# Kernel tuning notes

Hardware: AMD Instinct MI355X
Metric: run time of the kernel (lower is better)

Reference implementation:

```python
import jax, jax.numpy as jnp
import numpy as np

N = 100000     # total points
PBS = 500      # point_batch_size (hard-coded in module)
K = 100        # num_neighbors
KP = 15        # num_kernel_points
EPS = 1e-5


def _bn(x, g, b, axes):
    # torch BatchNorm in training mode: batch stats, biased variance
    m = jnp.mean(x, axis=axes, keepdims=True)
    v = jnp.var(x, axis=axes, keepdims=True)
    return (x - m) / jnp.sqrt(v + EPS) * g + b


def setup_inputs() -> dict:
    key = jax.random.key(0)
    ks = jax.random.split(key, 16)
    rn = lambda k, sh, s=1.0: jax.random.normal(k, sh, jnp.float32) * s
    return {
        "pts": rn(ks[0], (N, 3)),
        "normal": rn(ks[1], (N, 3)),
        "kp_points": rn(ks[2], (KP, 3)),
        "kp_weights": rn(ks[3], (KP, 3, 128), 0.3),
        "kp_sigma": jnp.float32(1.0),
        "conv1_w": rn(ks[4], (1024, 128), 128 ** -0.5),
        "conv1_b": rn(ks[5], (1024,), 0.02),
        "bn1_g": jnp.ones((1024,), jnp.float32),
        "bn1_b": jnp.zeros((1024,), jnp.float32),
        "fc1_w": rn(ks[6], (512, 1024), 1024 ** -0.5),
        "fc1_b": rn(ks[7], (512,), 0.02),
        "bn4_g": jnp.ones((512,), jnp.float32),
        "bn4_b": jnp.zeros((512,), jnp.float32),
        "fc2_w": rn(ks[8], (256, 512), 512 ** -0.5),
        "fc2_b": rn(ks[9], (256,), 0.02),
        "bn5_g": jnp.ones((256,), jnp.float32),
        "bn5_b": jnp.zeros((256,), jnp.float32),
        "fc3_w": rn(ks[10], (3, 256), 256 ** -0.5),
        "fc3_b": rn(ks[11], (3,), 0.02),
        "index": jax.random.randint(ks[12], (PBS,), 0, N, jnp.int32),
    }


def reference(pts, normal, kp_points, kp_weights, kp_sigma,
              conv1_w, conv1_b, bn1_g, bn1_b,
              fc1_w, fc1_b, bn4_g, bn4_b,
              fc2_w, fc2_b, bn5_g, bn5_b,
              fc3_w, fc3_b, index):
    sel = pts[index]                                               # [B,3]
    # L-inf pairwise distance and kNN (topk of -dist, as in the torch code)
    dist = jnp.max(jnp.abs(sel[:, None, :] - pts[None, :, :]), axis=-1)  # [B,N]
    _, nbr = jax.lax.top_k(-dist, K)                               # [B,K]
    rel = pts[nbr] - sel[:, None, :]                               # [B,K,3]

    # KPConv: gaussian weights vs kernel points, per-kernel-point linear map
    d2 = jnp.sum((rel[:, :, None, :] - kp_points[None, None]) ** 2, axis=-1)  # [B,K,KP]
    w = jnp.exp(-0.5 * d2 / (kp_sigma ** 2))
    wf = rel[:, :, None, :] * w[..., None]                         # [B,K,KP,3]
    h = jax.nn.relu(jnp.einsum('bnkc,kco->bno', wf, kp_weights))   # [B,K,128]

    # 1x1 conv 128->1024, relu then BN over (batch, points) per channel
    h = jnp.einsum('bnc,oc->bno', h, conv1_w) + conv1_b            # [B,K,1024]
    h = _bn(jax.nn.relu(h), bn1_g, bn1_b, (0, 1))
    feat = jnp.max(h, axis=1)                                      # [B,1024]

    feat = _bn(jax.nn.relu(feat @ fc1_w.T + fc1_b), bn4_g, bn4_b, (0,))
    feat = _bn(jax.nn.relu(feat @ fc2_w.T + fc2_b), bn5_g, bn5_b, (0,))
    feat = feat @ fc3_w.T + fc3_b                                  # [B,3]
    return feat, normal[index]
```

## Files before the change

### kernel.cpp

```cpp
#include <hip/hip_runtime.h>
#include <hip/hip_fp16.h>

#define NPTS 100000
#define NB 500
#define KNN 100
#define KPN 15
#define C1 128
#define C2 1024
#define C3 512
#define C4 256

#define G 64
#define NCELLS (G * G * G)
#define GB 5.0f
#define GINVH ((float)G / (2.f * GB))
#define CAND_CAP 2048

typedef _Float16 half8 __attribute__((ext_vector_type(8)));
typedef float f32x4 __attribute__((ext_vector_type(4)));

__device__ __forceinline__ int cell_coord(float x) {
  int c = (int)floorf((x + GB) * GINVH);
  return min(max(c, 0), G - 1);
}
__device__ __forceinline__ int cell_of(float x, float y, float z) {
  return (cell_coord(x) << 12) | (cell_coord(y) << 6) | cell_coord(z);
}

__global__ __launch_bounds__(256) void prep_kernel(
    const float* __restrict__ pts, const float* __restrict__ normal,
    const int* __restrict__ index, const float* __restrict__ w1,
    const float* __restrict__ kpw, const float* __restrict__ fc1w,
    float* __restrict__ sel, float* __restrict__ out2,
    __half* __restrict__ wh, __half* __restrict__ kpwT_hi,
    __half* __restrict__ kpwT_lo, __half* __restrict__ fwhi,
    __half* __restrict__ fwlo, unsigned* __restrict__ cnt) {
  int i = blockIdx.x * 256 + threadIdx.x;
  if (i < NB) {
    int ix = index[i];
    sel[i * 3 + 0] = pts[3 * ix + 0];
    sel[i * 3 + 1] = pts[3 * ix + 1];
    sel[i * 3 + 2] = pts[3 * ix + 2];
    out2[i * 3 + 0] = normal[3 * ix + 0];
    out2[i * 3 + 1] = normal[3 * ix + 1];
    out2[i * 3 + 2] = normal[3 * ix + 2];
  }
  if (i < C2 * C1) wh[i] = __float2half(w1[i]);
  if (i < 128 * 64) {
    int o = i >> 6, j = i & 63;
    float v = (j < 45) ? kpw[j * 128 + o] : 0.f;
    __half hi = __float2half_rn(v);
    kpwT_hi[i] = hi;
    kpwT_lo[i] = __float2half_rn(v - __half2float(hi));
  }
  if (i < C3 * C2) {
    float v = fc1w[i];
    __half hi = __float2half_rn(v);
    fwhi[i] = hi;
    fwlo[i] = __float2half_rn(v - __half2float(hi));
  }
  if (i < NPTS)
    atomicAdd(&cnt[cell_of(pts[3 * i], pts[3 * i + 1], pts[3 * i + 2])], 1u);
}

__global__ __launch_bounds__(256) void grid_scan1_kernel(
    const unsigned* __restrict__ cnt, unsigned* __restrict__ cursor,
    unsigned* __restrict__ chunktot) {
  const int tid = threadIdx.x;
  int base = blockIdx.x * 1024 + tid * 4;
  unsigned c0 = cnt[base], c1 = cnt[base + 1], c2 = cnt[base + 2],
           c3 = cnt[base + 3];
  unsigned tot = c0 + c1 + c2 + c3;
  __shared__ unsigned sb[256];
  sb[tid] = tot;
  __syncthreads();
  for (int off = 1; off < 256; off <<= 1) {
    unsigned add = (tid >= off) ? sb[tid - off] : 0u;
    __syncthreads();
    sb[tid] += add;
    __syncthreads();
  }
  unsigned excl = sb[tid] - tot;
  cursor[base] = excl;
  cursor[base + 1] = excl + c0;
  cursor[base + 2] = excl + c0 + c1;
  cursor[base + 3] = excl + c0 + c1 + c2;
  if (tid == 255) chunktot[blockIdx.x] = sb[255];
}

__global__ __launch_bounds__(256) void grid_scan2_kernel(
    const unsigned* __restrict__ chunktot, unsigned* __restrict__ chunkoff) {
  const int tid = threadIdx.x;
  unsigned v = chunktot[tid];
  __shared__ unsigned sb[256];
  sb[tid] = v;
  __syncthreads();
  for (int off = 1; off < 256; off <<= 1) {
    unsigned add = (tid >= off) ? sb[tid - off] : 0u;
    __syncthreads();
    sb[tid] += add;
    __syncthreads();
  }
  chunkoff[tid] = sb[tid] - v;
}

__global__ __launch_bounds__(256) void grid_scan3_kernel(
    unsigned* __restrict__ cursor, const unsigned* __restrict__ chunkoff) {
  unsigned off = chunkoff[blockIdx.x];
  int base = blockIdx.x * 1024 + threadIdx.x * 4;
#pragma unroll
  for (int j = 0; j < 4; ++j) cursor[base + j] += off;
}

__global__ __launch_bounds__(256) void grid_scatter_kernel(
    const float* __restrict__ pts, unsigned* __restrict__ cursor,
    float4* __restrict__ sorted) {
  int i = blockIdx.x * 256 + threadIdx.x;
  if (i >= NPTS) return;
  float x = pts[3 * i], y = pts[3 * i + 1], z = pts[3 * i + 2];
  unsigned pos = atomicAdd(&cursor[cell_of(x, y, z)], 1u);
  sorted[pos] = make_float4(x, y, z, __int_as_float(i));
}

__device__ __forceinline__ unsigned linf_bits(float px, float py, float pz,
                                              float sx, float sy, float sz) {
  float dx = fabsf(px - sx), dy = fabsf(py - sy), dz = fabsf(pz - sz);
  return __float_as_uint(fmaxf(fmaxf(dx, dy), dz));
}

__global__ __launch_bounds__(256) void knn_kernel(
    const float4* __restrict__ sorted, const unsigned* __restrict__ cnt,
    const unsigned* __restrict__ cursor,
    const float* __restrict__ sel, int* __restrict__ nbr) {
  const int b = blockIdx.x;
  const int tid = threadIdx.x;
  __shared__ unsigned cbits[CAND_CAP];
  __shared__ int cidx[CAND_CAP];
  __shared__ unsigned hist[4096];
  __shared__ unsigned scanbuf[256];
  __shared__ int s_total, s_m, s_mc, s_chunk;
  __shared__ unsigned s_excl, s_bub;

  const float qx = sel[b * 3 + 0], qy = sel[b * 3 + 1], qz = sel[b * 3 + 2];
  const int qcx = cell_coord(qx), qcy = cell_coord(qy), qcz = cell_coord(qz);

  if (tid == 0) s_total = 0;
  __syncthreads();
  int s = 1;
  int pxlo = 1, pxhi = 0, pylo = 1, pyhi = 0, pzlo = 1, pzhi = 0;
  int xlo, xhi, ylo, yhi, zlo, zhi;
  for (;;) {
    xlo = max(qcx - s, 0); xhi = min(qcx + s, G - 1);
    ylo = max(qcy - s, 0); yhi = min(qcy + s, G - 1);
    zlo = max(qcz - s, 0); zhi = min(qcz + s, G - 1);
    int nx = xhi - xlo + 1, ny = yhi - ylo + 1, nz = zhi - zlo + 1;
    int ncell = nx * ny * nz;
    unsigned local = 0;
    for (int ci = tid; ci < ncell; ci += 256) {
      int cz = ci % nz;
      int r = ci / nz;
      int cy = r % ny;
      int cx = r / ny;
      int ax = xlo + cx, ay = ylo + cy, az = zlo + cz;
      if (ax >= pxlo && ax <= pxhi && ay >= pylo && ay <= pyhi &&
          az >= pzlo && az <= pzhi)
        continue;
      local += cnt[(ax << 12) | (ay << 6) | az];
    }
#pragma unroll
    for (int off = 32; off; off >>= 1) local += __shfl_down(local, off);
    if ((tid & 63) == 0) atomicAdd(&s_total, (int)local);
    __syncthreads();
    if (s_total >= KNN || (xlo == 0 && ylo == 0 && zlo == 0 && xhi == G - 1 &&
                           yhi == G - 1 && zhi == G - 1))
      break;
    pxlo = xlo; pxhi = xhi; pylo = ylo; pyhi = yhi; pzlo = zlo; pzhi = zhi;
    ++s;
    __syncthreads();
  }

  if (tid == 0) s_m = 0;
  __syncthreads();
  {
    int nx = xhi - xlo + 1, ny = yhi - ylo + 1, nz = zhi - zlo + 1;
    int ncell = nx * ny * nz;
    for (int ci = tid; ci < ncell; ci += 256) {
      int cz = ci % nz;
      int r = ci / nz;
      int cy = r % ny;
      int cx = r / ny;
      int cell = ((xlo + cx) << 12) | ((ylo + cy) << 6) | (zlo + cz);
      unsigned end = cursor[cell];
      unsigned beg = end - cnt[cell];
      int k = (int)(end - beg);
      if (k > 0) {
        int e0 = atomicAdd(&s_m, k);
        for (unsigned p = beg; p < end; ++p, ++e0) {
          if (e0 < CAND_CAP) {
            float4 f = sorted[p];
            cbits[e0] = linf_bits(f.x, f.y, f.z, qx, qy, qz);
            cidx[e0] = __float_as_int(f.w);
          }
        }
      }
    }
  }
  __syncthreads();
  int m = s_m < CAND_CAP ? s_m : CAND_CAP;

  for (int j = tid; j < 4096; j += 256) hist[j] = 0;
  __syncthreads();
  for (int e = tid; e < m; e += 256) atomicAdd(&hist[cbits[e] >> 19], 1u);
  __syncthreads();
  unsigned csum = 0;
  {
    int c0 = tid * 16;
#pragma unroll
    for (int j = 0; j < 16; ++j) csum += hist[c0 + j];
  }
  scanbuf[tid] = csum;
  __syncthreads();
  for (int off = 1; off < 256; off <<= 1) {
    unsigned add = (tid >= off) ? scanbuf[tid - off] : 0u;
    __syncthreads();
    scanbuf[tid] += add;
    __syncthreads();
  }
  {
    unsigned incl = scanbuf[tid], excl = incl - csum;
    if (excl < KNN && KNN <= incl) {
      s_chunk = tid;
      s_excl = excl;
    }
  }
  __syncthreads();
  if (tid == 0) {
    unsigned cum = s_excl;
    int bin = s_chunk * 16;
    while (cum + hist[bin] < KNN) {
      cum += hist[bin];
      ++bin;
    }
    s_bub = (unsigned)(bin + 1) << 19;
  }
  __syncthreads();

  const unsigned bub = s_bub;
  const float dub = __uint_as_float(bub);
  if (tid == 0) s_mc = 0;
  __syncthreads();
  {
    int xlo2 = min(max((int)floorf((qx - dub + GB) * GINVH), 0), G - 1);
    int xhi2 = min(max((int)floorf((qx + dub + GB) * GINVH), 0), G - 1);
    int ylo2 = min(max((int)floorf((qy - dub + GB) * GINVH), 0), G - 1);
    int yhi2 = min(max((int)floorf((qy + dub + GB) * GINVH), 0), G - 1);
    int zlo2 = min(max((int)floorf((qz - dub + GB) * GINVH), 0), G - 1);
    int zhi2 = min(max((int)floorf((qz + dub + GB) * GINVH), 0), G - 1);
    int nx = xhi2 - xlo2 + 1, ny = yhi2 - ylo2 + 1, nz = zhi2 - zlo2 + 1;
    int ncell = nx * ny * nz;
    for (int ci = tid; ci < ncell; ci += 256) {
      int cz = ci % nz;
      int r = ci / nz;
      int cy = r % ny;
      int cx = r / ny;
      int cell = ((xlo2 + cx) << 12) | ((ylo2 + cy) << 6) | (zlo2 + cz);
      unsigned end = cursor[cell];
      unsigned beg = end - cnt[cell];
      for (unsigned p = beg; p < end; ++p) {
        float4 f = sorted[p];
        unsigned bits = linf_bits(f.x, f.y, f.z, qx, qy, qz);
        if (bits < bub) {
          int e = atomicAdd(&s_mc, 1);
          if (e < CAND_CAP) {
            cbits[e] = bits;
            cidx[e] = __float_as_int(f.w);
          }
        }
      }
    }
  }
  __syncthreads();
  int mc = s_mc < CAND_CAP ? s_mc : CAND_CAP;

  for (int c = tid; c < mc; c += 256) {
    unsigned bc = cbits[c];
    int ic = cidx[c];
    int rank = 0;
    for (int j = 0; j < mc; ++j) {
      unsigned bj = cbits[j];
      rank += (bj < bc || (bj == bc && cidx[j] < ic)) ? 1 : 0;
    }
    if (rank < KNN) nbr[b * KNN + rank] = ic;
  }
}

__global__ __launch_bounds__(512) void kpconv_conv1_kernel(
    const float* __restrict__ pts, const float* __restrict__ sel,
    const int* __restrict__ nbr, const float* __restrict__ kp_points,
    const __half* __restrict__ kpwT_hi, const __half* __restrict__ kpwT_lo,
    const float* __restrict__ kp_sigma, const __half* __restrict__ wh,
    const float* __restrict__ bias, float* __restrict__ featmax,
    float* __restrict__ featmin, float* __restrict__ bnsum,
    float* __restrict__ bnsq) {
  const int b = blockIdx.x;
  const int tid = threadIdx.x;
  const int wave = tid >> 6, lane = tid & 63;
  const int lr = lane & 15, quad = lane >> 4;

  __shared__ __align__(16) char smem[71168];
  __half* As_hi = (__half*)smem;
  __half* As_lo = As_hi + 112 * 72;
  __half* Bs_hi = As_lo + 112 * 72;
  __half* Bs_lo = Bs_hi + 128 * 72;
  float* rel = (float*)(Bs_lo + 128 * 72);
  float* kpp = rel + 100 * 4;
  __half* Hs = (__half*)smem;
  __half* Ws = Hs + 112 * 136;

  for (int i = tid; i < 128 * 8; i += 512) {
    int row = i >> 3, seg = i & 7;
    *(float4*)&Bs_hi[row * 72 + seg * 8] =
        *(const float4*)&kpwT_hi[row * 64 + seg * 8];
    *(float4*)&Bs_lo[row * 72 + seg * 8] =
        *(const float4*)&kpwT_lo[row * 64 + seg * 8];
  }
  {
    float4 z = make_float4(0.f, 0.f, 0.f, 0.f);
    for (int i = tid; i < 112 * 8; i += 512) {
      int row = i >> 3, seg = i & 7;
      *(float4*)&As_hi[row * 72 + seg * 8] = z;
      *(float4*)&As_lo[row * 72 + seg * 8] = z;
    }
  }
  if (tid < 45) kpp[tid] = kp_points[tid];
  if (tid < 100) {
    int idx = nbr[b * KNN + tid];
    rel[tid * 4 + 0] = pts[3 * idx + 0] - sel[b * 3 + 0];
    rel[tid * 4 + 1] = pts[3 * idx + 1] - sel[b * 3 + 1];
    rel[tid * 4 + 2] = pts[3 * idx + 2] - sel[b * 3 + 2];
  }
  __syncthreads();

  const float sg = kp_sigma[0];
  const float inv2s2 = -0.5f / (sg * sg);
  for (int i = tid; i < 100 * KPN; i += 512) {
    int k = i / KPN, p = i - k * KPN;
    float rx = rel[k * 4 + 0] - kpp[p * 3 + 0];
    float ry = rel[k * 4 + 1] - kpp[p * 3 + 1];
    float rz = rel[k * 4 + 2] - kpp[p * 3 + 2];
    float w = expf(inv2s2 * (rx * rx + ry * ry + rz * rz));
#pragma unroll
    for (int c = 0; c < 3; ++c) {
      float a = rel[k * 4 + c] * w;
      __half hi = __float2half_rn(a);
      As_hi[k * 72 + p * 3 + c] = hi;
      As_lo[k * 72 + p * 3 + c] = __float2half_rn(a - __half2float(hi));
    }
  }
  __syncthreads();

  f32x4 acc1[7];
#pragma unroll
  for (int m = 0; m < 7; ++m) acc1[m] = (f32x4)(0.f);
#pragma unroll
  for (int s = 0; s < 2; ++s) {
    int boff = (wave * 16 + lr) * 72 + s * 32 + quad * 8;
    half8 bhi = *(const half8*)&Bs_hi[boff];
    half8 blo = *(const half8*)&Bs_lo[boff];
#pragma unroll
    for (int m = 0; m < 7; ++m) {
      int aoff = (m * 16 + lr) * 72 + s * 32 + quad * 8;
      half8 ahi = *(const half8*)&As_hi[aoff];
      half8 alo = *(const half8*)&As_lo[aoff];
      acc1[m] = __builtin_amdgcn_mfma_f32_16x16x32_f16(ahi, bhi, acc1[m], 0, 0, 0);
      acc1[m] = __builtin_amdgcn_mfma_f32_16x16x32_f16(ahi, blo, acc1[m], 0, 0, 0);
      acc1[m] = __builtin_amdgcn_mfma_f32_16x16x32_f16(alo, bhi, acc1[m], 0, 0, 0);
    }
  }
  __syncthreads();

  {
    int col = wave * 16 + lr;
#pragma unroll
    for (int m = 0; m < 7; ++m)
#pragma unroll
      for (int r = 0; r < 4; ++r) {
        int row = m * 16 + quad * 4 + r;
        Hs[row * 136 + col] = __float2half_rn(fmaxf(acc1[m][r], 0.f));
      }
  }

  for (int c = 0; c < 8; ++c) {
    __syncthreads();
    for (int i = tid; i < 128 * 16; i += 512) {
      int row = i >> 4, seg = i & 15;
      *(float4*)&Ws[row * 136 + seg * 8] =
          *(const float4*)&wh[(c * 128 + row) * 128 + seg * 8];
    }
    __syncthreads();

    f32x4 acc2[7];
#pragma unroll
    for (int m = 0; m < 7; ++m) acc2[m] = (f32x4)(0.f);
#pragma unroll
    for (int s = 0; s < 4; ++s) {
      half8 bfrag =
          *(const half8*)&Ws[(wave * 16 + lr) * 136 + s * 32 + quad * 8];
#pragma unroll
      for (int m = 0; m < 7; ++m) {
        half8 afrag =
            *(const half8*)&Hs[(m * 16 + lr) * 136 + s * 32 + quad * 8];
        acc2[m] = __builtin_amdgcn_mfma_f32_16x16x32_f16(afrag, bfrag,
                                                         acc2[m], 0, 0, 0);
      }
    }

    {
      int col = c * 128 + wave * 16 + lr;
      float bv = bias[col];
      float pmax = -1e30f, pmin = 1e30f, psum = 0.f, psq = 0.f;
#pragma unroll
      for (int m = 0; m < 7; ++m)
#pragma unroll
        for (int r = 0; r < 4; ++r) {
          int row = m * 16 + quad * 4 + r;
          if (row < 100) {
            float y = fmaxf(acc2[m][r] + bv, 0.f);
            pmax = fmaxf(pmax, y);
            pmin = fminf(pmin, y);
            psum += y;
            psq += y * y;
          }
        }
      pmax = fmaxf(pmax, __shfl_xor(pmax, 16));
      pmax = fmaxf(pmax, __shfl_xor(pmax, 32));
      pmin = fminf(pmin, __shfl_xor(pmin, 16));
      pmin = fminf(pmin, __shfl_xor(pmin, 32));
      psum += __shfl_xor(psum, 16);
      psum += __shfl_xor(psum, 32);
      psq += __shfl_xor(psq, 16);
      psq += __shfl_xor(psq, 32);
      if (quad == 0) {
        featmax[b * C2 + col] = pmax;
        featmin[b * C2 + col] = pmin;
        atomicAdd(&bnsum[col], psum);
        atomicAdd(&bnsq[col], psq);
      }
    }
  }
}

__global__ __launch_bounds__(256) void bn1half_kernel(
    const float* __restrict__ featmax, const float* __restrict__ featmin,
    const float* __restrict__ bnsum, const float* __restrict__ bnsq,
    const float* __restrict__ g, const float* __restrict__ bb,
    __half* __restrict__ Xhi, __half* __restrict__ Xlo) {
  int idx = blockIdx.x * 256 + threadIdx.x;
  if (idx >= NB * C2) return;
  int o = idx & (C2 - 1);
  const float invn = 1.f / (float)(NB * KNN);
  float m = bnsum[o] * invn;
  float v = bnsq[o] * invn - m * m;
  float a = g[o] / sqrtf(v + 1e-5f);
  float x = (a >= 0.f) ? featmax[idx] : featmin[idx];
  float y = (x - m) * a + bb[o];
  __half hi = __float2half_rn(y);
  Xhi[idx] = hi;
  Xlo[idx] = __float2half_rn(y - __half2float(hi));
}

__global__ __launch_bounds__(256) void fc1_mfma_kernel(
    const __half* __restrict__ Xhi, const __half* __restrict__ Xlo,
    const __half* __restrict__ Whi, const __half* __restrict__ Wlo,
    const float* __restrict__ bias, float* __restrict__ yraw,
    float* __restrict__ s, float* __restrict__ sq) {
  const int r0 = blockIdx.x * 64;
  const int n0 = blockIdx.y * 64;
  const int tid = threadIdx.x;
  const int wave = tid >> 6, lane = tid & 63;
  const int lr = lane & 15, quad = lane >> 4;
  __shared__ __half Xs_hi[64 * 72], Xs_lo[64 * 72];
  __shared__ __half Ws_hi[64 * 72], Ws_lo[64 * 72];

  f32x4 acc[4];
#pragma unroll
  for (int m = 0; m < 4; ++m) acc[m] = (f32x4)(0.f);

  for (int kc = 0; kc < C2; kc += 64) {
    __syncthreads();
    for (int i = tid; i < 64 * 8; i += 256) {
      int row = i >> 3, seg = i & 7;
      int gr = r0 + row;
      float4 vhi = make_float4(0.f, 0.f, 0.f, 0.f), vlo = vhi;
      if (gr < NB) {
        vhi = *(const float4*)&Xhi[gr * C2 + kc + seg * 8];
        vlo = *(const float4*)&Xlo[gr * C2 + kc + seg * 8];
      }
      *(float4*)&Xs_hi[row * 72 + seg * 8] = vhi;
      *(float4*)&Xs_lo[row * 72 + seg * 8] = vlo;
      *(float4*)&Ws_hi[row * 72 + seg * 8] =
          *(const float4*)&Whi[(n0 + row) * C2 + kc + seg * 8];
      *(float4*)&Ws_lo[row * 72 + seg * 8] =
          *(const float4*)&Wlo[(n0 + row) * C2 + kc + seg * 8];
    }
    __syncthreads();

#pragma unroll
    for (int s2 = 0; s2 < 2; ++s2) {
      int boff = (wave * 16 + lr) * 72 + s2 * 32 + quad * 8;
      half8 bhi = *(const half8*)&Ws_hi[boff];
      half8 blo = *(const half8*)&Ws_lo[boff];
#pragma unroll
      for (int m = 0; m < 4; ++m) {
        int aoff = (m * 16 + lr) * 72 + s2 * 32 + quad * 8;
        half8 ahi = *(const half8*)&Xs_hi[aoff];
        half8 alo = *(const half8*)&Xs_lo[aoff];
        acc[m] = __builtin_amdgcn_mfma_f32_16x16x32_f16(ahi, bhi, acc[m], 0, 0, 0);
        acc[m] = __builtin_amdgcn_mfma_f32_16x16x32_f16(ahi, blo, acc[m], 0, 0, 0);
        acc[m] = __builtin_amdgcn_mfma_f32_16x16x32_f16(alo, bhi, acc[m], 0, 0, 0);
      }
    }
  }

  {
    int col = n0 + wave * 16 + lr;
    float bv = bias[col];
    float psum = 0.f, psq = 0.f;
#pragma unroll
    for (int m = 0; m < 4; ++m)
#pragma unroll
      for (int r = 0; r < 4; ++r) {
        int row = r0 + m * 16 + quad * 4 + r;
        if (row < NB) {
          float y = fmaxf(acc[m][r] + bv, 0.f);
          yraw[row * C3 + col] = y;
          psum += y;
          psq += y * y;
        }
      }
    psum += __shfl_xor(psum, 16);
    psum += __shfl_xor(psum, 32);
    psq += __shfl_xor(psq, 16);
    psq += __shfl_xor(psq, 32);
    if (quad == 0) {
      atomicAdd(&s[col], psum);
      atomicAdd(&sq[col], psq);
    }
  }
}

__global__ __launch_bounds__(256) void fc2_kernel(
    const float* __restrict__ x,
    const float* __restrict__ bnsum, const float* __restrict__ bnsq,
    const float* __restrict__ g, const float* __restrict__ bb,
    const float* __restrict__ w,
    const float* __restrict__ bias, float* __restrict__ yraw,
    float* __restrict__ s, float* __restrict__ sq) {
  const int r0 = blockIdx.x * 4;
  const int n0 = blockIdx.y * 64;
  const int tid = threadIdx.x;
  const int col = tid >> 2;
  const int row = tid & 3;
  __shared__ float xs[4][516];
  __shared__ float ws[64][132];
  __shared__ float amul[C3], badd[C3];
  const float invn = 1.f / (float)NB;
  for (int o = tid; o < C3; o += 256) {
    float m = bnsum[o] * invn;
    float v = bnsq[o] * invn - m * m;
    float a = g[o] / sqrtf(v + 1e-5f);
    amul[o] = a;
    badd[o] = bb[o] - m * a;
  }
  __syncthreads();
  for (int f = tid; f < C3; f += 256) {
    int rr = f >> 7, kq = (f & 127) * 4;
    float4 xv = *(const float4*)&x[(r0 + rr) * C3 + kq];
    float4 o4;
    o4.x = xv.x * amul[kq + 0] + badd[kq + 0];
    o4.y = xv.y * amul[kq + 1] + badd[kq + 1];
    o4.z = xv.z * amul[kq + 2] + badd[kq + 2];
    o4.w = xv.w * amul[kq + 3] + badd[kq + 3];
    *(float4*)&xs[rr][kq] = o4;
  }
  float acc = 0.f;
  for (int kc = 0; kc < C3; kc += 128) {
    __syncthreads();
#pragma unroll
    for (int i = 0; i < 8; ++i) {
      int f = tid + i * 256;
      int cr = f >> 5, kq = (f & 31) * 4;
      *(float4*)&ws[cr][kq] = *(const float4*)&w[(n0 + cr) * C3 + kc + kq];
    }
    __syncthreads();
    for (int kk = 0; kk < 128; kk += 4) {
      float4 xv = *(float4*)&xs[row][kc + kk];
      float4 wv = *(float4*)&ws[col][kk];
      acc += xv.x * wv.x + xv.y * wv.y + xv.z * wv.z + xv.w * wv.w;
    }
  }
  float y = fmaxf(acc + bias[n0 + col], 0.f);
  yraw[(r0 + row) * C4 + n0 + col] = y;
  float ys = y, y2 = y * y;
  ys += __shfl_xor(ys, 1); y2 += __shfl_xor(y2, 1);
  ys += __shfl_xor(ys, 2); y2 += __shfl_xor(y2, 2);
  if (row == 0) {
    atomicAdd(&s[n0 + col], ys);
    atomicAdd(&sq[n0 + col], y2);
  }
}

__global__ __launch_bounds__(256) void fc3_kernel(
    const float* __restrict__ x,
    const float* __restrict__ bnsum, const float* __restrict__ bnsq,
    const float* __restrict__ g, const float* __restrict__ bb,
    const float* __restrict__ w, const float* __restrict__ bias,
    float* __restrict__ out) {
  const int tid = threadIdx.x;
  __shared__ float pmul[C4], padd[C4];
  {
    const float invn = 1.f / (float)NB;
    float m = bnsum[tid] * invn;
    float v = bnsq[tid] * invn - m * m;
    float a = g[tid] / sqrtf(v + 1e-5f);
    pmul[tid] = a;
    padd[tid] = bb[tid] - m * a;
  }
  __syncthreads();
  int idx = blockIdx.x * 256 + tid;
  if (idx >= NB * 3) return;
  int b = idx / 3, o = idx % 3;
  float acc = 0.f;
  for (int k = 0; k < C4; ++k)
    acc += (x[b * C4 + k] * pmul[k] + padd[k]) * w[o * C4 + k];
  out[idx] = acc + bias[o];
}

extern "C" void kernel_launch(void* const* d_in, const int* in_sizes, int n_in,
                              void* d_out, int out_size, void* d_ws,
                              size_t ws_size, hipStream_t stream) {
  const float* pts = (const float*)d_in[0];
  const float* normal = (const float*)d_in[1];
  const float* kp_points = (const float*)d_in[2];
  const float* kp_weights = (const float*)d_in[3];
  const float* kp_sigma = (const float*)d_in[4];
  const float* conv1_w = (const float*)d_in[5];
  const float* conv1_b = (const float*)d_in[6];
  const float* bn1_g = (const float*)d_in[7];
  const float* bn1_b = (const float*)d_in[8];
  const float* fc1_w = (const float*)d_in[9];
  const float* fc1_b = (const float*)d_in[10];
  const float* bn4_g = (const float*)d_in[11];
  const float* bn4_b = (const float*)d_in[12];
  const float* fc2_w = (const float*)d_in[13];
  const float* fc2_b = (const float*)d_in[14];
  const float* bn5_g = (const float*)d_in[15];
  const float* bn5_b = (const float*)d_in[16];
  const float* fc3_w = (const float*)d_in[17];
  const float* fc3_b = (const float*)d_in[18];
  const int* index = (const int*)d_in[19];
  float* out = (float*)d_out;

  char* p = (char*)d_ws;
  auto carve = [&](size_t bytes) {
    void* r = (void*)p;
    p += (bytes + 255) & ~(size_t)255;
    return r;
  };
  float* sel = (float*)carve(NB * 3 * 4);
  int* nbr = (int*)carve(NB * KNN * 4);
  __half* wh = (__half*)carve((size_t)C2 * C1 * 2);
  __half* kpwT_hi = (__half*)carve((size_t)128 * 64 * 2);
  __half* kpwT_lo = (__half*)carve((size_t)128 * 64 * 2);
  __half* fwhi = (__half*)carve((size_t)C3 * C2 * 2);
  __half* fwlo = (__half*)carve((size_t)C3 * C2 * 2);
  __half* Xhi = (__half*)carve((size_t)NB * C2 * 2);
  __half* Xlo = (__half*)carve((size_t)NB * C2 * 2);
  float* featmax = (float*)carve(NB * C2 * 4);
  float* featmin = (float*)carve(NB * C2 * 4);
  float* f2raw = (float*)carve(NB * C3 * 4);
  float* f3raw = (float*)carve(NB * C4 * 4);
  float* stats = (float*)carve((2 * C2 + 2 * C3 + 2 * C4) * 4);
  float* bnsum = stats;
  float* bnsq = stats + C2;
  float* s4 = stats + 2 * C2;
  float* sq4 = s4 + C3;
  float* s5 = sq4 + C3;
  float* sq5 = s5 + C4;
  unsigned* cellcnt = (unsigned*)carve((size_t)NCELLS * 4);
  unsigned* cellcur = (unsigned*)carve((size_t)NCELLS * 4);
  unsigned* chunktot = (unsigned*)carve(256 * 4);
  unsigned* chunkoff = (unsigned*)carve(256 * 4);
  float4* sortedpts = (float4*)carve((size_t)NPTS * 16);

  hipMemsetAsync(stats, 0, (2 * C2 + 2 * C3 + 2 * C4) * 4, stream);
  hipMemsetAsync(cellcnt, 0, (size_t)NCELLS * 4, stream);

  prep_kernel<<<(C3 * C2 + 255) / 256, 256, 0, stream>>>(
      pts, normal, index, conv1_w, kp_weights, fc1_w, sel, out + NB * 3, wh,
      kpwT_hi, kpwT_lo, fwhi, fwlo, cellcnt);
  grid_scan1_kernel<<<256, 256, 0, stream>>>(cellcnt, cellcur, chunktot);
  grid_scan2_kernel<<<1, 256, 0, stream>>>(chunktot, chunkoff);
  grid_scan3_kernel<<<256, 256, 0, stream>>>(cellcur, chunkoff);
  grid_scatter_kernel<<<(NPTS + 255) / 256, 256, 0, stream>>>(pts, cellcur,
                                                              sortedpts);
  knn_kernel<<<NB, 256, 0, stream>>>(sortedpts, cellcnt, cellcur, sel, nbr);
  kpconv_conv1_kernel<<<NB, 512, 0, stream>>>(
      pts, sel, nbr, kp_points, kpwT_hi, kpwT_lo, kp_sigma, wh, conv1_b,
      featmax, featmin, bnsum, bnsq);
  bn1half_kernel<<<(NB * C2 + 255) / 256, 256, 0, stream>>>(
      featmax, featmin, bnsum, bnsq, bn1_g, bn1_b, Xhi, Xlo);
  fc1_mfma_kernel<<<dim3(8, 8), 256, 0, stream>>>(Xhi, Xlo, fwhi, fwlo, fc1_b,
                                                  f2raw, s4, sq4);
  fc2_kernel<<<dim3(125, C4 / 64), 256, 0, stream>>>(
      f2raw, s4, sq4, bn4_g, bn4_b, fc2_w, fc2_b, f3raw, s5, sq5);
  fc3_kernel<<<(NB * 3 + 255) / 256, 256, 0, stream>>>(
      f3raw, s5, sq5, bn5_g, bn5_b, fc3_w, fc3_b, out);
}
```

Measured before the change: 266.2 us.

## Keep conv1 A fragments in registers and prefetch weights directly from global

The conv1 GEMM stage used to stage each 128-row weight chunk through shared memory behind two block barriers per chunk. It now loads all H fragments into registers once and reads each wave's B fragments straight from global memory, double-buffering the next chunk in registers while the current one computes. This removes the LDS round trip and the per-chunk barriers. In exchange it raises register pressure (28 half8 A fragments plus two sets of B fragments), and the launch bounds now request 2 blocks per CU.

Result: faster. 255.6 us (-4.0%).

```diff
diff --git a/kernel.cpp b/kernel.cpp
--- a/kernel.cpp
+++ b/kernel.cpp
@@ -294,7 +294,7 @@
   }
 }
 
-__global__ __launch_bounds__(512) void kpconv_conv1_kernel(
+__global__ __launch_bounds__(512, 2) void kpconv_conv1_kernel(
     const float* __restrict__ pts, const float* __restrict__ sel,
     const int* __restrict__ nbr, const float* __restrict__ kp_points,
     const __half* __restrict__ kpwT_hi, const __half* __restrict__ kpwT_lo,
@@ -315,7 +315,6 @@
   float* rel = (float*)(Bs_lo + 128 * 72);
   float* kpp = rel + 100 * 4;
   __half* Hs = (__half*)smem;
-  __half* Ws = Hs + 112 * 136;
 
   for (int i = tid; i < 128 * 8; i += 512) {
     int row = i >> 3, seg = i & 7;
@@ -389,34 +388,42 @@
         Hs[row * 136 + col] = __float2half_rn(fmaxf(acc1[m][r], 0.f));
       }
   }
+  __syncthreads();
+
+  half8 afr[4][7];
+#pragma unroll
+  for (int s = 0; s < 4; ++s)
+#pragma unroll
+    for (int m = 0; m < 7; ++m)
+      afr[s][m] = *(const half8*)&Hs[(m * 16 + lr) * 136 + s * 32 + quad * 8];
+
+  const int wrow = wave * 16 + lr;
+  half8 bcur[4];
+#pragma unroll
+  for (int s = 0; s < 4; ++s)
+    bcur[s] = *(const half8*)&wh[wrow * 128 + s * 32 + quad * 8];
 
   for (int c = 0; c < 8; ++c) {
-    __syncthreads();
-    for (int i = tid; i < 128 * 16; i += 512) {
-      int row = i >> 4, seg = i & 15;
-      *(float4*)&Ws[row * 136 + seg * 8] =
-          *(const float4*)&wh[(c * 128 + row) * 128 + seg * 8];
-    }
-    __syncthreads();
+    half8 bnxt[4];
+    if (c + 1 < 8) {
+#pragma unroll
+      for (int s = 0; s < 4; ++s)
+        bnxt[s] = *(const half8*)&wh[((c + 1) * 128 + wrow) * 128 + s * 32 +
+                                     quad * 8];
+    }
 
     f32x4 acc2[7];
 #pragma unroll
     for (int m = 0; m < 7; ++m) acc2[m] = (f32x4)(0.f);
 #pragma unroll
-    for (int s = 0; s < 4; ++s) {
-      half8 bfrag =
-          *(const half8*)&Ws[(wave * 16 + lr) * 136 + s * 32 + quad * 8];
-#pragma unroll
-      for (int m = 0; m < 7; ++m) {
-        half8 afrag =
-            *(const half8*)&Hs[(m * 16 + lr) * 136 + s * 32 + quad * 8];
-        acc2[m] = __builtin_amdgcn_mfma_f32_16x16x32_f16(afrag, bfrag,
+    for (int s = 0; s < 4; ++s)
+#pragma unroll
+      for (int m = 0; m < 7; ++m)
+        acc2[m] = __builtin_amdgcn_mfma_f32_16x16x32_f16(afr[s][m], bcur[s],
                                                          acc2[m], 0, 0, 0);
-      }
-    }
 
     {
-      int col = c * 128 + wave * 16 + lr;
+      int col = c * 128 + wrow;
       float bv = bias[col];
       float pmax = -1e30f, pmin = 1e30f, psum = 0.f, psq = 0.f;
 #pragma unroll
@@ -447,6 +454,8 @@
         atomicAdd(&bnsq[col], psq);
       }
     }
+#pragma unroll
+    for (int s = 0; s < 4; ++s) bcur[s] = bnxt[s];
   }
 }
 
```
